# Optimization experiments

Hardware: AMD Instinct MI355X
Metric: run time of the kernel (lower is better)

The kernel has to match this reference:

```python
import jax, jax.numpy as jnp
import numpy as np

DIM = 768
HEADS = 12
DIM_HEAD = DIM // HEADS
FACTOR = DIM_HEAD ** (-0.5)
B, T = 4, 2048


def setup_inputs() -> dict:
    key = jax.random.key(0)
    k1, k2, k3 = jax.random.split(key, 3)
    x = jax.random.normal(k1, (B, T, DIM), dtype=jnp.float32)
    # VarianceScaling-like init scale for linear weights
    W_qkv = jax.random.normal(k2, (DIM, 3 * DIM), dtype=jnp.float32) * (DIM ** -0.5)
    W_out = jax.random.normal(k3, (DIM, DIM), dtype=jnp.float32) * (DIM ** -0.5)
    return {"x": x, "W_qkv": W_qkv, "W_out": W_out}


def reference(x, W_qkv, W_out):
    b, t, _ = x.shape
    qkv = x @ W_qkv  # [b, t, 3*dim]
    # einops 'b t (d k h) -> k b h t d' with k=3, h=HEADS: d slowest, k middle, h fastest
    qkv = qkv.reshape(b, t, DIM_HEAD, 3, HEADS)
    qkv = jnp.transpose(qkv, (3, 0, 4, 1, 2))  # [3, b, h, t, d]
    q, k, v = qkv[0], qkv[1], qkv[2]
    # scaled dot-product attention, full [b,h,t,t] scores as in the original
    scores = jnp.einsum('bhid,bhjd->bhij', q, k) * FACTOR
    attn = jax.nn.softmax(scores, axis=-1)
    out = jnp.einsum('bhij,bhjd->bhid', attn, v)  # [b, h, t, d]
    # 'b h t d -> b t (h d)'
    out = jnp.transpose(out, (0, 2, 1, 3)).reshape(b, t, HEADS * DIM_HEAD)
    return out @ W_out
```

## Files before the change

kernel.cpp:

```cpp
#include <hip/hip_runtime.h>
#include <hip/hip_bf16.h>

#define DIM    768
#define HEADS  12
#define DHEAD  64
#define BATCH  4
#define SEQ    2048
#define NROW   (BATCH * SEQ)
#define QKVN   (3 * DIM)
#define FACTOR 0.125f
#define QSCALE 0.18033688011112042f

typedef __attribute__((ext_vector_type(8))) short short8;
typedef __attribute__((ext_vector_type(4))) float floatx4;

__device__ __forceinline__ floatx4 mfma16(short8 a, short8 b, floatx4 c) {
    return __builtin_amdgcn_mfma_f32_16x16x32_bf16(a, b, c, 0, 0, 0);
}

__device__ __forceinline__ void glds16(const void* g, void* l) {
    __builtin_amdgcn_global_load_lds((const __attribute__((address_space(1))) void*)g,
                                     (__attribute__((address_space(3))) void*)l,
                                     16, 0, 0);
}

__device__ __forceinline__ short rne16(float f) {
    unsigned u = __builtin_bit_cast(unsigned, f);
    return (short)((u + 0x7fffu + ((u >> 16) & 1u)) >> 16);
}
__device__ __forceinline__ unsigned pack2(float lo, float hi) {
    unsigned ul = __builtin_bit_cast(unsigned, lo);
    unsigned uh = __builtin_bit_cast(unsigned, hi);
    ul = (ul + 0x7fffu + ((ul >> 16) & 1u)) >> 16;
    uh = (uh + 0x7fffu + ((uh >> 16) & 1u)) & 0xffff0000u;
    return ul | uh;
}

__device__ __forceinline__ int swz8(int row, int col) {
    return (row << 6) + ((((col >> 3) ^ row) & 7) << 3) + (col & 7);
}

__global__ __launch_bounds__(256) void conv_bf16(const float* __restrict__ x,
                                                 short* __restrict__ xb) {
    int g = blockIdx.x * 256 + threadIdx.x;
    float4 v = ((const float4*)x)[g];
    uint2 o;
    o.x = pack2(v.x, v.y);
    o.y = pack2(v.z, v.w);
    ((uint2*)xb)[g] = o;
}

__global__ __launch_bounds__(256) void transpose_w(const float* __restrict__ W,
                                                   short* __restrict__ Wt,
                                                   int K, int N, int permute) {
    __shared__ short T[32][33];
    int n0 = blockIdx.x * 32, k0 = blockIdx.y * 32;
    int c = threadIdx.x & 31, r0 = threadIdx.x >> 5;
    for (int r = r0; r < 32; r += 8)
        T[r][c] = rne16(W[(size_t)(k0 + r) * N + n0 + c]);
    __syncthreads();
    for (int r = r0; r < 32; r += 8) {
        int n = n0 + r;
        int np;
        if (permute) {
            int d = n / 36, rem = n - d * 36;
            int which = rem / 12, h = rem - which * 12;
            np = which * 768 + h * 64 + d;
        } else {
            np = n;
        }
        Wt[(size_t)np * K + k0 + c] = T[c][r];
    }
}

__global__ __launch_bounds__(256) void gemm_qkv(const short* __restrict__ A,
                                                const short* __restrict__ Bt,
                                                short* __restrict__ Qo,
                                                short* __restrict__ Ko,
                                                short* __restrict__ Vto) {
    __shared__ short As[128 * 64];
    __shared__ short Bs[128 * 64];
    const int tid = threadIdx.x;
    const int lane = tid & 63, wave = tid >> 6;
    const int l15 = lane & 15, quad = lane >> 4;

    const int flat = blockIdx.x;
    const int xcd = flat & 7;
    const int local = flat >> 3;
    const int mloc = local & 7, nloc = local >> 3;
    const int m0 = (xcd * 8 + mloc) * 128;
    const int n0 = nloc * 128;

    const int wm = (wave >> 1) * 64, wn = (wave & 1) * 64;
    const int r8 = wave * 8 + (lane >> 3);
    const int c8 = lane & 7;
    const int sc = ((c8 ^ (r8 & 7)) << 3);

    floatx4 acc[4][4] = {};
    for (int k0 = 0; k0 < DIM; k0 += 64) {
#pragma unroll
        for (int i = 0; i < 4; ++i) {
            int row = i * 32 + r8;
            glds16(&A[(size_t)(m0 + row) * DIM + k0 + sc], &As[(size_t)(i * 32 + wave * 8) * 64]);
            glds16(&Bt[(size_t)(n0 + row) * DIM + k0 + sc], &Bs[(size_t)(i * 32 + wave * 8) * 64]);
        }
        __syncthreads();
#pragma unroll
        for (int ks = 0; ks < 2; ++ks) {
            short8 a[4], b[4];
#pragma unroll
            for (int mt = 0; mt < 4; ++mt)
                a[mt] = *(const short8*)&As[swz8(wm + mt * 16 + l15, ks * 32 + quad * 8)];
#pragma unroll
            for (int nt = 0; nt < 4; ++nt)
                b[nt] = *(const short8*)&Bs[swz8(wn + nt * 16 + l15, ks * 32 + quad * 8)];
#pragma unroll
            for (int mt = 0; mt < 4; ++mt)
#pragma unroll
                for (int nt = 0; nt < 4; ++nt)
                    acc[mt][nt] = mfma16(a[mt], b[nt], acc[mt][nt]);
        }
        __syncthreads();
    }

    const int sn = n0 + wn;
    const int which = sn / 768;
    const int h = (sn - which * 768) >> 6;
    const int bb = (m0 + wm) >> 11;
    const int tbase = (m0 + wm) & 2047;
    const size_t tilebase = ((size_t)(bb * HEADS + h) * 32 + (tbase >> 6)) * 4096;

    if (which != 2) {
        short* dst = (which == 0) ? Qo : Ko;
        const float scale = (which == 0) ? QSCALE : 1.0f;
#pragma unroll
        for (int mt = 0; mt < 4; ++mt)
#pragma unroll
            for (int nt = 0; nt < 4; ++nt) {
                int d = nt * 16 + l15;
#pragma unroll
                for (int r = 0; r < 4; ++r) {
                    int tl = mt * 16 + quad * 4 + r;
                    dst[tilebase + swz8(tl, d)] = rne16(acc[mt][nt][r] * scale);
                }
            }
    } else {
        short* vld = ((wave < 2) ? As : Bs) + (wave & 1) * 4096;
#pragma unroll
        for (int mt = 0; mt < 4; ++mt)
#pragma unroll
            for (int nt = 0; nt < 4; ++nt) {
                int d = nt * 16 + l15;
                int tl = mt * 16 + quad * 4;
                int chunk = (tl >> 3) ^ (d & 7);
                int addr = (d << 6) + (chunk << 3) + (tl & 7);
                uint2 pk;
                pk.x = pack2(acc[mt][nt][0], acc[mt][nt][1]);
                pk.y = pack2(acc[mt][nt][2], acc[mt][nt][3]);
                *(uint2*)&vld[addr] = pk;
            }
    }
    __syncthreads();
    if (which == 2) {
        short* vld = ((wave < 2) ? As : Bs) + (wave & 1) * 4096;
#pragma unroll
        for (int i = 0; i < 8; ++i) {
            int c = (i * 64 + lane) * 8;
            *(uint4*)&Vto[tilebase + c] = *(const uint4*)&vld[c];
        }
    }
}

__global__ __launch_bounds__(512, 6) void attn_mfma(const short* __restrict__ Q,
                                                    const short* __restrict__ K,
                                                    const short* __restrict__ Vt,
                                                    short* __restrict__ O) {
    __shared__ __align__(16) short buf[8192];
    __shared__ __align__(16) short Ps[8192];
    __shared__ float Lx[256];

    const int tid = threadIdx.x;
    const int lane = tid & 63, wave = tid >> 6;
    const int l15 = lane & 15, quad = lane >> 4;
    const int pair = wave >> 1, sh = wave & 1;
    const int flat = blockIdx.x;
    const int xcd = flat & 7, li = flat >> 3;
    const int bh = xcd + (li % 6) * 8;
    const int q0 = (li / 6) * 128;
    const size_t base = (size_t)bh * SEQ * DHEAD;
    short* Ks = buf;
    short* Vs = buf + 4096;
    short* Pp = Ps + pair * 2048;
    const int lane8 = lane * 8;

    {
        size_t qtb = base + (size_t)(q0 >> 6) * 4096;
#pragma unroll
        for (int i = 0; i < 2; ++i)
            glds16(&Q[qtb + (size_t)(i * 8 + wave) * 512 + lane8],
                   &buf[(i * 8 + wave) * 512]);
    }
    __syncthreads();
    short8 qf[2][2];
#pragma unroll
    for (int mt = 0; mt < 2; ++mt)
#pragma unroll
        for (int ks = 0; ks < 2; ++ks)
            qf[mt][ks] = *(const short8*)&buf[swz8(pair * 32 + mt * 16 + l15,
                                                   ks * 32 + quad * 8)];
    __syncthreads();

    floatx4 o[2][2] = {};
    float lsum[2] = {0.f, 0.f};

    for (int j0 = 0; j0 < SEQ; j0 += 64) {
        size_t ktb = base + (size_t)(j0 >> 6) * 4096 + wave * 512 + lane8;
        glds16(&K[ktb], &Ks[wave * 512]);
        glds16(&Vt[ktb], &Vs[wave * 512]);
        __syncthreads();

        floatx4 sa[2][2] = {};
#pragma unroll
        for (int ks = 0; ks < 2; ++ks) {
            short8 kf0 = *(const short8*)&Ks[swz8(sh * 32 + l15, ks * 32 + quad * 8)];
            short8 kf1 = *(const short8*)&Ks[swz8(sh * 32 + 16 + l15, ks * 32 + quad * 8)];
            sa[0][0] = mfma16(kf0, qf[0][ks], sa[0][0]);
            sa[0][1] = mfma16(kf1, qf[0][ks], sa[0][1]);
            sa[1][0] = mfma16(kf0, qf[1][ks], sa[1][0]);
            sa[1][1] = mfma16(kf1, qf[1][ks], sa[1][1]);
        }

#pragma unroll
        for (int mt = 0; mt < 2; ++mt)
#pragma unroll
            for (int kt = 0; kt < 2; ++kt) {
                float p0 = __builtin_amdgcn_exp2f(sa[mt][kt][0]);
                float p1 = __builtin_amdgcn_exp2f(sa[mt][kt][1]);
                float p2 = __builtin_amdgcn_exp2f(sa[mt][kt][2]);
                float p3 = __builtin_amdgcn_exp2f(sa[mt][kt][3]);
                lsum[mt] += (p0 + p1) + (p2 + p3);
                uint2 pk;
                pk.x = pack2(p0, p1);
                pk.y = pack2(p2, p3);
                *(uint2*)&Pp[swz8(mt * 16 + l15, sh * 32 + kt * 16 + quad * 4)] = pk;
            }
        __syncthreads();

#pragma unroll
        for (int ks = 0; ks < 2; ++ks) {
            short8 a0 = *(const short8*)&Pp[swz8(l15, ks * 32 + quad * 8)];
            short8 a1 = *(const short8*)&Pp[swz8(16 + l15, ks * 32 + quad * 8)];
            short8 b0 = *(const short8*)&Vs[swz8(sh * 32 + l15, ks * 32 + quad * 8)];
            short8 b1 = *(const short8*)&Vs[swz8(sh * 32 + 16 + l15, ks * 32 + quad * 8)];
            o[0][0] = mfma16(a0, b0, o[0][0]);
            o[0][1] = mfma16(a0, b1, o[0][1]);
            o[1][0] = mfma16(a1, b0, o[1][0]);
            o[1][1] = mfma16(a1, b1, o[1][1]);
        }
        __syncthreads();
    }

    float r0 = lsum[0], r1 = lsum[1];
    r0 += __shfl_xor(r0, 16); r0 += __shfl_xor(r0, 32);
    r1 += __shfl_xor(r1, 16); r1 += __shfl_xor(r1, 32);
    if (quad == 0) {
        Lx[pair * 64 + sh * 32 + l15] = r0;
        Lx[pair * 64 + sh * 32 + 16 + l15] = r1;
    }
    __syncthreads();
    float inv0 = 1.f / (r0 + Lx[pair * 64 + (sh ^ 1) * 32 + l15]);
    float inv1 = 1.f / (r1 + Lx[pair * 64 + (sh ^ 1) * 32 + 16 + l15]);

    const int b = bh / HEADS, h = bh - b * HEADS;
#pragma unroll
    for (int r = 0; r < 4; ++r) {
        float iv0 = __shfl(inv0, quad * 4 + r);
        float iv1 = __shfl(inv1, quad * 4 + r);
#pragma unroll
        for (int mt = 0; mt < 2; ++mt) {
            int t = q0 + pair * 32 + mt * 16 + quad * 4 + r;
            float iv = mt ? iv1 : iv0;
            size_t rowo = ((size_t)(b * SEQ + t)) * DIM + h * DHEAD + sh * 32;
            O[rowo + l15] = rne16(o[mt][0][r] * iv);
            O[rowo + 16 + l15] = rne16(o[mt][1][r] * iv);
        }
    }
}

__global__ __launch_bounds__(256) void gemm_out(const short* __restrict__ A,
                                                const short* __restrict__ Bt,
                                                float* __restrict__ out) {
    __shared__ short As[128 * 64];
    __shared__ short Bs[128 * 64];
    const int tid = threadIdx.x;
    const int lane = tid & 63, wave = tid >> 6;
    const int l15 = lane & 15, quad = lane >> 4;
    const int m0 = blockIdx.y * 128, n0 = blockIdx.x * 128;
    const int wm = (wave >> 1) * 64, wn = (wave & 1) * 64;
    const int r8 = wave * 8 + (lane >> 3);
    const int sc = (((lane & 7) ^ (r8 & 7)) << 3);

    floatx4 acc[4][4] = {};
    for (int k0 = 0; k0 < DIM; k0 += 64) {
#pragma unroll
        for (int i = 0; i < 4; ++i) {
            int row = i * 32 + r8;
            glds16(&A[(size_t)(m0 + row) * DIM + k0 + sc], &As[(size_t)(i * 32 + wave * 8) * 64]);
            glds16(&Bt[(size_t)(n0 + row) * DIM + k0 + sc], &Bs[(size_t)(i * 32 + wave * 8) * 64]);
        }
        __syncthreads();
#pragma unroll
        for (int ks = 0; ks < 2; ++ks) {
            short8 a[4], b[4];
#pragma unroll
            for (int mt = 0; mt < 4; ++mt)
                a[mt] = *(const short8*)&As[swz8(wm + mt * 16 + l15, ks * 32 + quad * 8)];
#pragma unroll
            for (int nt = 0; nt < 4; ++nt)
                b[nt] = *(const short8*)&Bs[swz8(wn + nt * 16 + l15, ks * 32 + quad * 8)];
#pragma unroll
            for (int mt = 0; mt < 4; ++mt)
#pragma unroll
                for (int nt = 0; nt < 4; ++nt)
                    acc[mt][nt] = mfma16(a[mt], b[nt], acc[mt][nt]);
        }
        __syncthreads();
    }

#pragma unroll
    for (int mt = 0; mt < 4; ++mt)
#pragma unroll
        for (int nt = 0; nt < 4; ++nt)
#pragma unroll
            for (int r = 0; r < 4; ++r) {
                int m = m0 + wm + mt * 16 + quad * 4 + r;
                int n = n0 + wn + nt * 16 + l15;
                out[(size_t)m * DIM + n] = acc[mt][nt][r];
            }
}

extern "C" void kernel_launch(void* const* d_in, const int* in_sizes, int n_in,
                              void* d_out, int out_size, void* d_ws, size_t ws_size,
                              hipStream_t stream) {
    const float* x    = (const float*)d_in[0];
    const float* Wqkv = (const float*)d_in[1];
    const float* Wout = (const float*)d_in[2];
    float* out = (float*)d_out;

    const size_t NE = (size_t)NROW * DIM;
    short* xb  = (short*)d_ws;
    short* Wqt = xb + NE;
    short* Wot = Wqt + (size_t)QKVN * DIM;
    short* Qw  = Wot + (size_t)DIM * DIM;
    short* Kw  = Qw + NE;
    short* Vtw = Kw + NE;

    conv_bf16<<<NE / 4 / 256, 256, 0, stream>>>(x, xb);
    transpose_w<<<dim3(QKVN / 32, DIM / 32), 256, 0, stream>>>(Wqkv, Wqt, DIM, QKVN, 1);
    transpose_w<<<dim3(DIM / 32, DIM / 32), 256, 0, stream>>>(Wout, Wot, DIM, DIM, 0);
    gemm_qkv<<<8 * 8 * 18, 256, 0, stream>>>(xb, Wqt, Qw, Kw, Vtw);
    attn_mfma<<<768, 512, 0, stream>>>(Qw, Kw, Vtw, xb);
    gemm_out<<<dim3(DIM / 128, NROW / 128), 256, 0, stream>>>(xb, Wot, out);
}
```

Baseline: 225.9 us.

## Merge prep kernels, fold Q scale into weights, swap MFMA operands for vector stores

Combines the x conversion and both weight transposes into a single prep launch. The Q scale is now applied to the bf16 weights, which removes the per-element multiply in the QKV epilogue. MFMA operands are swapped for the Q/K tiles and for the output GEMM, so each lane holds four contiguous columns and can write packed 8-byte bf16 or 16-byte float stores instead of scalar ones. Scaling the weights after bf16 rounding adds a second rounding step, which slightly changes numerics.

```diff
diff --git a/kernel.cpp b/kernel.cpp
--- a/kernel.cpp
+++ b/kernel.cpp
@@ -40,36 +40,47 @@
     return (row << 6) + ((((col >> 3) ^ row) & 7) << 3) + (col & 7);
 }
 
-__global__ __launch_bounds__(256) void conv_bf16(const float* __restrict__ x,
-                                                 short* __restrict__ xb) {
-    int g = blockIdx.x * 256 + threadIdx.x;
-    float4 v = ((const float4*)x)[g];
-    uint2 o;
-    o.x = pack2(v.x, v.y);
-    o.y = pack2(v.z, v.w);
-    ((uint2*)xb)[g] = o;
-}
-
-__global__ __launch_bounds__(256) void transpose_w(const float* __restrict__ W,
-                                                   short* __restrict__ Wt,
-                                                   int K, int N, int permute) {
+__global__ __launch_bounds__(256) void prep(const float* __restrict__ x,
+                                            short* __restrict__ xb,
+                                            const float* __restrict__ Wqkv,
+                                            short* __restrict__ Wqt,
+                                            const float* __restrict__ Wout,
+                                            short* __restrict__ Wot) {
     __shared__ short T[32][33];
-    int n0 = blockIdx.x * 32, k0 = blockIdx.y * 32;
+    int blk = blockIdx.x;
+    if (blk < 6144) {
+        int g = blk * 256 + threadIdx.x;
+        float4 v = ((const float4*)x)[g];
+        uint2 o;
+        o.x = pack2(v.x, v.y);
+        o.y = pack2(v.z, v.w);
+        ((uint2*)xb)[g] = o;
+        return;
+    }
+    blk -= 6144;
+    const float* W;
+    short* Wt;
+    int N, permute, bx, by;
+    if (blk < 1728) { W = Wqkv; Wt = Wqt; N = QKVN; permute = 1; bx = blk % 72; by = blk / 72; }
+    else { blk -= 1728; W = Wout; Wt = Wot; N = DIM; permute = 0; bx = blk % 24; by = blk / 24; }
+
+    int n0 = bx * 32, k0 = by * 32;
     int c = threadIdx.x & 31, r0 = threadIdx.x >> 5;
     for (int r = r0; r < 32; r += 8)
         T[r][c] = rne16(W[(size_t)(k0 + r) * N + n0 + c]);
     __syncthreads();
     for (int r = r0; r < 32; r += 8) {
         int n = n0 + r;
-        int np;
+        int np = n;
+        float scale = 1.0f;
         if (permute) {
             int d = n / 36, rem = n - d * 36;
             int which = rem / 12, h = rem - which * 12;
             np = which * 768 + h * 64 + d;
-        } else {
-            np = n;
-        }
-        Wt[(size_t)np * K + k0 + c] = T[c][r];
+            if (which == 0) scale = QSCALE;
+        }
+        float v = __bfloat162float(__hip_bfloat16_raw{(unsigned short)T[c][r]});
+        Wt[(size_t)np * DIM + k0 + c] = (scale == 1.0f) ? T[c][r] : rne16(v * scale);
     }
 }
 
@@ -96,6 +107,10 @@
     const int c8 = lane & 7;
     const int sc = ((c8 ^ (r8 & 7)) << 3);
 
+    const int sn = n0 + wn;
+    const int which = sn / 768;
+    const bool swapAB = (which != 2);
+
     floatx4 acc[4][4] = {};
     for (int k0 = 0; k0 < DIM; k0 += 64) {
 #pragma unroll
@@ -114,17 +129,23 @@
 #pragma unroll
             for (int nt = 0; nt < 4; ++nt)
                 b[nt] = *(const short8*)&Bs[swz8(wn + nt * 16 + l15, ks * 32 + quad * 8)];
-#pragma unroll
-            for (int mt = 0; mt < 4; ++mt)
-#pragma unroll
-                for (int nt = 0; nt < 4; ++nt)
-                    acc[mt][nt] = mfma16(a[mt], b[nt], acc[mt][nt]);
-        }
-        __syncthreads();
-    }
-
-    const int sn = n0 + wn;
-    const int which = sn / 768;
+            if (swapAB) {
+#pragma unroll
+                for (int mt = 0; mt < 4; ++mt)
+#pragma unroll
+                    for (int nt = 0; nt < 4; ++nt)
+                        acc[mt][nt] = mfma16(b[nt], a[mt], acc[mt][nt]);
+            } else {
+#pragma unroll
+                for (int mt = 0; mt < 4; ++mt)
+#pragma unroll
+                    for (int nt = 0; nt < 4; ++nt)
+                        acc[mt][nt] = mfma16(a[mt], b[nt], acc[mt][nt]);
+            }
+        }
+        __syncthreads();
+    }
+
     const int h = (sn - which * 768) >> 6;
     const int bb = (m0 + wm) >> 11;
     const int tbase = (m0 + wm) & 2047;
@@ -132,17 +153,16 @@
 
     if (which != 2) {
         short* dst = (which == 0) ? Qo : Ko;
-        const float scale = (which == 0) ? QSCALE : 1.0f;
 #pragma unroll
         for (int mt = 0; mt < 4; ++mt)
 #pragma unroll
             for (int nt = 0; nt < 4; ++nt) {
-                int d = nt * 16 + l15;
-#pragma unroll
-                for (int r = 0; r < 4; ++r) {
-                    int tl = mt * 16 + quad * 4 + r;
-                    dst[tilebase + swz8(tl, d)] = rne16(acc[mt][nt][r] * scale);
-                }
+                int tl = mt * 16 + l15;
+                int d0 = nt * 16 + quad * 4;
+                uint2 pk;
+                pk.x = pack2(acc[mt][nt][0], acc[mt][nt][1]);
+                pk.y = pack2(acc[mt][nt][2], acc[mt][nt][3]);
+                *(uint2*)&dst[tilebase + swz8(tl, d0)] = pk;
             }
     } else {
         short* vld = ((wave < 2) ? As : Bs) + (wave & 1) * 4096;
@@ -322,7 +342,7 @@
             for (int mt = 0; mt < 4; ++mt)
 #pragma unroll
                 for (int nt = 0; nt < 4; ++nt)
-                    acc[mt][nt] = mfma16(a[mt], b[nt], acc[mt][nt]);
+                    acc[mt][nt] = mfma16(b[nt], a[mt], acc[mt][nt]);
         }
         __syncthreads();
     }
@@ -330,13 +350,11 @@
 #pragma unroll
     for (int mt = 0; mt < 4; ++mt)
 #pragma unroll
-        for (int nt = 0; nt < 4; ++nt)
-#pragma unroll
-            for (int r = 0; r < 4; ++r) {
-                int m = m0 + wm + mt * 16 + quad * 4 + r;
-                int n = n0 + wn + nt * 16 + l15;
-                out[(size_t)m * DIM + n] = acc[mt][nt][r];
-            }
+        for (int nt = 0; nt < 4; ++nt) {
+            int m = m0 + wm + mt * 16 + l15;
+            int n = n0 + wn + nt * 16 + quad * 4;
+            *(floatx4*)&out[(size_t)m * DIM + n] = acc[mt][nt];
+        }
 }
 
 extern "C" void kernel_launch(void* const* d_in, const int* in_sizes, int n_in,
@@ -355,9 +373,7 @@
     short* Kw  = Qw + NE;
     short* Vtw = Kw + NE;
 
-    conv_bf16<<<NE / 4 / 256, 256, 0, stream>>>(x, xb);
-    transpose_w<<<dim3(QKVN / 32, DIM / 32), 256, 0, stream>>>(Wqkv, Wqt, DIM, QKVN, 1);
-    transpose_w<<<dim3(DIM / 32, DIM / 32), 256, 0, stream>>>(Wout, Wot, DIM, DIM, 0);
+    prep<<<6144 + 1728 + 576, 256, 0, stream>>>(x, xb, Wqkv, Wqt, Wout, Wot);
     gemm_qkv<<<8 * 8 * 18, 256, 0, stream>>>(xb, Wqt, Qw, Kw, Vtw);
     attn_mfma<<<768, 512, 0, stream>>>(Qw, Kw, Vtw, xb);
     gemm_out<<<dim3(DIM / 128, NROW / 128), 256, 0, stream>>>(xb, Wot, out);
```

After: 219.0 us. -3.1%, faster.
